# Performance work log

Hardware: AMD Instinct MI355X
Metric: run time of the kernel (lower is better)

Reference implementation:

```python
import jax, jax.numpy as jnp
import numpy as np

NUM_USERS = 100000
NUM_ITEMS = 50000
N_NODES = NUM_USERS + NUM_ITEMS
D = 64
N_LAYERS = 3
E = 2000000
B = 1024
ALPHA_PREF = 1.0


def setup_inputs() -> dict:
    key = jax.random.key(0)
    k1, k2, k3, k4 = jax.random.split(key, 4)
    embed = jax.random.normal(k1, (N_NODES, D), dtype=jnp.float32) * 0.1
    edge_index = jax.random.randint(k2, (2, E), 0, N_NODES, dtype=jnp.int32)
    users = jax.random.randint(k3, (B,), 0, NUM_USERS, dtype=jnp.int32)
    items = jax.random.randint(k4, (B,), 0, NUM_ITEMS, dtype=jnp.int32)
    return {"embed": embed, "edge_index": edge_index, "users": users, "items": items}


def _lightgcn_propagate(x, row, col, norm):
    # message: norm * x[row] (x_j = source), aggregated (add) at col (target)
    msg = norm[:, None] * x[row]                      # [E, D]
    return jnp.zeros_like(x).at[col].add(msg)         # [N, D]


def reference(embed, edge_index, users, items):
    row, col = edge_index[0], edge_index[1]
    n = embed.shape[0]
    # degree normalization (depends only on edge_index; same every layer)
    deg = jnp.zeros((n,), jnp.float32).at[row].add(1.0)
    deg_inv = jnp.clip(deg, 1.0, None) ** -0.5
    norm = deg_inv[row] * deg_inv[col]                # [E]

    x = embed
    for _ in range(N_LAYERS):
        x = _lightgcn_propagate(x, row, col, norm)

    u_emb = x[users]                                  # [B, D]
    i_emb = x[items + NUM_USERS]                      # [B, D]

    # mask = (row == users[:,None]) flattened selection of col; edge e is
    # selected once per batch element b with users[b] == row[e] -> multiplicity
    cnt = jnp.zeros((n,), jnp.float32).at[users].add(1.0)
    mult = cnt[row]                                   # [E] selection multiplicity

    # PreferenceShapley surrogate: softmax over selected neighbor embeddings
    # of alpha_pref * <neigh_emb, mean(u_emb)>, flattened over the batch.
    context = u_emb.mean(0)                           # [D]
    neigh = x[col]                                    # [E, D]
    logits = ALPHA_PREF * (neigh @ context)           # [E]
    masked = jnp.where(mult > 0, logits, -jnp.inf)
    mx = jnp.max(masked)
    ew = mult * jnp.exp(logits - mx)                  # [E] weighted exp (0 where unselected)
    z = jnp.clip(ew.sum(), 1e-12, None)
    neigh_aggr = (ew[:, None] * neigh).sum(0) / z     # [D]

    score = (u_emb * i_emb).sum(-1) + u_emb @ neigh_aggr  # [B]
    return jax.nn.sigmoid(score)
```

## Files before the change

kernel.cpp:

```cpp
#include <hip/hip_runtime.h>
#include <float.h>
#include <math.h>

#define NUM_USERS 100000
#define NUM_ITEMS 50000
#define NNODES    150000
#define DIM       64
#define NEDGE     2000000
#define BATCH     1024
#define SEL_CAP   (1 << 18)
#define LOGIT_BLOCKS 512

#define SLICES   1024
#define EPS      1956
#define NBUK     293
#define BCAP     8192
#define SCAP     16
#define OVF_CAP  4096

__device__ __forceinline__ float wave_sum64(float v) {
    #pragma unroll
    for (int off = 32; off > 0; off >>= 1) v += __shfl_xor(v, off, 64);
    return v;
}

__device__ __forceinline__ float bf2f(unsigned short s) {
    return __uint_as_float(((unsigned int)s) << 16);
}
__device__ __forceinline__ unsigned short f2bf(float f) {
    unsigned int u = __float_as_uint(f);
    return (unsigned short)((u + 0x7fffu + ((u >> 16) & 1u)) >> 16);
}


__global__ __launch_bounds__(512) void sort_kernel(
        const int* __restrict__ row, const int* __restrict__ col,
        const int* __restrict__ ucnt,
        unsigned char* __restrict__ cntC8, unsigned char* __restrict__ cntR8,
        unsigned int* __restrict__ midC2, unsigned short* __restrict__ midR2,
        uint2* __restrict__ ovfC, unsigned int* __restrict__ ovfR,
        int* __restrict__ novfC_g, int* __restrict__ novfR_g,
        int* __restrict__ n_sel, int* __restrict__ sel_col, float* __restrict__ sel_w) {
    __shared__ unsigned int hc[NBUK], hr[NBUK];
    __shared__ unsigned int   stC[NBUK * SCAP];
    __shared__ unsigned short stR[NBUK * SCAP];
    __shared__ int lcnt, lbase;
    __shared__ int2 buf[256];
    int blk = blockIdx.x, t = threadIdx.x;
    for (int i = t; i < NBUK; i += 512) { hc[i] = 0; hr[i] = 0; }
    if (t == 0) lcnt = 0;
    __syncthreads();
    int e0 = blk * EPS;
    int e1 = e0 + EPS; if (e1 > NEDGE) e1 = NEDGE;
    for (int base = e0 + t * 4; base < e1; base += 2048) {
        if (base + 4 <= e1) {
            int4 r4 = *(const int4*)(row + base);
            int4 c4 = *(const int4*)(col + base);
            #pragma unroll
            for (int q = 0; q < 4; ++q) {
                int c = (q == 0) ? c4.x : (q == 1) ? c4.y : (q == 2) ? c4.z : c4.w;
                int r = (q == 0) ? r4.x : (q == 1) ? r4.y : (q == 2) ? r4.z : r4.w;
                int bc = c >> 9;
                unsigned int kc = atomicAdd(&hc[bc], 1u);
                unsigned int v = ((unsigned int)(c & 511) << 18) | (unsigned int)r;
                if (kc < SCAP) stC[bc * SCAP + kc] = v;
                else { int i = atomicAdd(novfC_g, 1); if (i < OVF_CAP) ovfC[i] = make_uint2((unsigned int)bc, v); }
                int br = r >> 9;
                unsigned int kr = atomicAdd(&hr[br], 1u);
                if (kr < SCAP) stR[br * SCAP + kr] = (unsigned short)(r & 511);
                else { int i = atomicAdd(novfR_g, 1); if (i < OVF_CAP) ovfR[i] = ((unsigned int)br << 9) | (unsigned int)(r & 511); }
                int u = ucnt[r];
                if (u > 0) { int i = atomicAdd(&lcnt, 1); if (i < 256) buf[i] = make_int2(c, u); }
            }
        } else {
            for (int e = base; e < e1; ++e) {
                int r = row[e], c = col[e];
                int bc = c >> 9;
                unsigned int kc = atomicAdd(&hc[bc], 1u);
                unsigned int v = ((unsigned int)(c & 511) << 18) | (unsigned int)r;
                if (kc < SCAP) stC[bc * SCAP + kc] = v;
                else { int i = atomicAdd(novfC_g, 1); if (i < OVF_CAP) ovfC[i] = make_uint2((unsigned int)bc, v); }
                int br = r >> 9;
                unsigned int kr = atomicAdd(&hr[br], 1u);
                if (kr < SCAP) stR[br * SCAP + kr] = (unsigned short)(r & 511);
                else { int i = atomicAdd(novfR_g, 1); if (i < OVF_CAP) ovfR[i] = ((unsigned int)br << 9) | (unsigned int)(r & 511); }
                int u = ucnt[r];
                if (u > 0) { int i = atomicAdd(&lcnt, 1); if (i < 256) buf[i] = make_int2(c, u); }
            }
        }
    }
    __syncthreads();
    for (int j = t; j < NBUK * SCAP; j += 512) {
        int b = j >> 4, k = j & (SCAP - 1);
        unsigned int cc = hc[b]; if (cc > SCAP) cc = SCAP;
        if ((unsigned int)k < cc)
            midC2[(size_t)b * (SLICES * SCAP) + blk * SCAP + k] = stC[j];
        unsigned int cr = hr[b]; if (cr > SCAP) cr = SCAP;
        if ((unsigned int)k < cr)
            midR2[(size_t)b * (SLICES * SCAP) + blk * SCAP + k] = stR[j];
    }
    if (t < NBUK) {
        unsigned int cc = hc[t]; if (cc > SCAP) cc = SCAP;
        unsigned int cr = hr[t]; if (cr > SCAP) cr = SCAP;
        cntC8[(size_t)blk * NBUK + t] = (unsigned char)cc;
        cntR8[(size_t)blk * NBUK + t] = (unsigned char)cr;
    }
    if (t == 0) {
        int c = lcnt; c = c < 256 ? c : 256;
        lbase = atomicAdd(n_sel, c);
    }
    __syncthreads();
    int c = lcnt; c = c < 256 ? c : 256;
    int b = lbase;
    for (int i = t; i < c; i += 512) {
        int o = b + i;
        if (o < SEL_CAP) { sel_col[o] = buf[i].x; sel_w[o] = (float)buf[i].y; }
    }
}


__global__ __launch_bounds__(1024) void bfinal_kernel(
        const unsigned int* __restrict__ midC2, const unsigned char* __restrict__ cntC8,
        const unsigned short* __restrict__ midR2, const unsigned char* __restrict__ cntR8,
        const uint2* __restrict__ ovfC, const unsigned int* __restrict__ ovfR,
        const int* __restrict__ novfC_g, const int* __restrict__ novfR_g,
        const float4* __restrict__ embed,
        int* __restrict__ rptr, int* __restrict__ rend, int* __restrict__ src_sorted,
        float* __restrict__ dinv, float* __restrict__ dinv2,
        uint2* __restrict__ y0) {
    __shared__ int cnt[512], sm[512], cur[512];
    __shared__ unsigned char lcC[SLICES], lcR[SLICES];
    __shared__ float dinvL[512];
    int b = blockIdx.x, t = threadIdx.x;
    if (t < SLICES) {
        lcC[t] = cntC8[(size_t)t * NBUK + b];
        lcR[t] = cntR8[(size_t)t * NBUK + b];
    }
    if (t < 512) cnt[t] = 0;
    __syncthreads();
    size_t cbase = (size_t)b * (SLICES * SCAP);
    for (int j = t; j < SLICES * SCAP; j += 1024) {
        if ((unsigned int)(j & (SCAP - 1)) < (unsigned int)lcC[j >> 4])
            atomicAdd(&cnt[midC2[cbase + j] >> 18], 1);
    }
    int noC = *novfC_g; if (noC > OVF_CAP) noC = OVF_CAP;
    for (int i = t; i < noC; i += 1024)
        if ((int)ovfC[i].x == b) atomicAdd(&cnt[ovfC[i].y >> 18], 1);
    __syncthreads();
    if (t < 512) sm[t] = cnt[t];
    __syncthreads();
    for (int off = 1; off < 512; off <<= 1) {
        int v = 0;
        if (t < 512 && t >= off) v = sm[t - off];
        __syncthreads();
        if (t < 512) sm[t] += v;
        __syncthreads();
    }
    int s0 = b * BCAP;
    if (t < 512) {
        int excl = s0 + sm[t] - cnt[t];
        int n = b * 512 + t;
        if (n < NNODES) { rptr[n] = excl; rend[n] = s0 + sm[t]; }
        cur[t] = excl;
    }
    if (b == 0 && t < 16) y0[(size_t)NNODES * 16 + t] = make_uint2(0u, 0u);
    __syncthreads();
    for (int j = t; j < SLICES * SCAP; j += 1024) {
        if ((unsigned int)(j & (SCAP - 1)) < (unsigned int)lcC[j >> 4]) {
            unsigned int v = midC2[cbase + j];
            int dst = atomicAdd(&cur[v >> 18], 1);
            src_sorted[dst] = (int)(v & 0x3FFFFu);
        }
    }
    for (int i = t; i < noC; i += 1024)
        if ((int)ovfC[i].x == b) {
            unsigned int v = ovfC[i].y;
            int dst = atomicAdd(&cur[v >> 18], 1);
            src_sorted[dst] = (int)(v & 0x3FFFFu);
        }
    __syncthreads();
    if (t < 512) cnt[t] = 0;
    __syncthreads();
    for (int j = t; j < SLICES * SCAP; j += 1024) {
        if ((unsigned int)(j & (SCAP - 1)) < (unsigned int)lcR[j >> 4])
            atomicAdd(&cnt[midR2[cbase + j]], 1);
    }
    int noR = *novfR_g; if (noR > OVF_CAP) noR = OVF_CAP;
    for (int i = t; i < noR; i += 1024) {
        unsigned int pv = ovfR[i];
        if ((int)(pv >> 9) == b) atomicAdd(&cnt[pv & 511u], 1);
    }
    __syncthreads();
    if (t < 512) {
        int n = b * 512 + t;
        if (n < NNODES) {
            float d = fmaxf((float)cnt[t], 1.0f);
            float di = rsqrtf(d);
            dinv[n] = di; dinv2[n] = 1.0f / d;
            dinvL[t] = di;
        }
    }
    __syncthreads();
    int nbase = b * 512;
    int nmax = NNODES - nbase; if (nmax > 512) nmax = 512;
    if (nmax < 0) nmax = 0;
    for (int i = t; i < nmax * 16; i += 1024) {
        int ln = i >> 4, slot = i & 15;
        float d = dinvL[ln];
        float4 v = embed[(size_t)(nbase + ln) * 16 + slot];
        unsigned int w0 = (unsigned int)f2bf(v.x * d) | ((unsigned int)f2bf(v.y * d) << 16);
        unsigned int w1 = (unsigned int)f2bf(v.z * d) | ((unsigned int)f2bf(v.w * d) << 16);
        y0[(size_t)(nbase + ln) * 16 + slot] = make_uint2(w0, w1);
    }
}


#define ACC8(V) do { \
    a0 += __uint_as_float((V).x << 16); a1 += __uint_as_float((V).x & 0xffff0000u); \
    a2 += __uint_as_float((V).y << 16); a3 += __uint_as_float((V).y & 0xffff0000u); \
    a4 += __uint_as_float((V).z << 16); a5 += __uint_as_float((V).z & 0xffff0000u); \
    a6 += __uint_as_float((V).w << 16); a7 += __uint_as_float((V).w & 0xffff0000u); \
} while (0)

__device__ __forceinline__ void prop_node(
        const uint4* __restrict__ x_in, uint4* __restrict__ x_out,
        const int* __restrict__ ptr, const int* __restrict__ rend,
        const int* __restrict__ src,
        const float* __restrict__ scale, int node, int sl) {
    int i = ptr[node], e = rend[node];
    float sc = scale[node];
    float a0 = 0.f, a1 = 0.f, a2 = 0.f, a3 = 0.f;
    float a4 = 0.f, a5 = 0.f, a6 = 0.f, a7 = 0.f;
    int p0, p1, p2, p3;
    if (i + 4 <= e) { p0 = src[i]; p1 = src[i + 1]; p2 = src[i + 2]; p3 = src[i + 3]; }
    while (i + 8 <= e) {
        uint4 w0 = x_in[p0 * 8 + sl];
        uint4 w1 = x_in[p1 * 8 + sl];
        uint4 w2 = x_in[p2 * 8 + sl];
        uint4 w3 = x_in[p3 * 8 + sl];
        p0 = src[i + 4]; p1 = src[i + 5]; p2 = src[i + 6]; p3 = src[i + 7];
        i += 4;
        ACC8(w0); ACC8(w1); ACC8(w2); ACC8(w3);
    }
    if (i + 4 <= e) {
        uint4 w0 = x_in[p0 * 8 + sl];
        uint4 w1 = x_in[p1 * 8 + sl];
        uint4 w2 = x_in[p2 * 8 + sl];
        uint4 w3 = x_in[p3 * 8 + sl];
        i += 4;
        ACC8(w0); ACC8(w1); ACC8(w2); ACC8(w3);
    }
    if (i < e) {
        int q0 = src[i];
        int q1 = (i + 1 < e) ? src[i + 1] : NNODES;
        int q2 = (i + 2 < e) ? src[i + 2] : NNODES;
        uint4 w0 = x_in[q0 * 8 + sl];
        uint4 w1 = x_in[q1 * 8 + sl];
        uint4 w2 = x_in[q2 * 8 + sl];
        ACC8(w0); ACC8(w1); ACC8(w2);
    }
    uint4 o;
    o.x = (unsigned int)f2bf(a0 * sc) | ((unsigned int)f2bf(a1 * sc) << 16);
    o.y = (unsigned int)f2bf(a2 * sc) | ((unsigned int)f2bf(a3 * sc) << 16);
    o.z = (unsigned int)f2bf(a4 * sc) | ((unsigned int)f2bf(a5 * sc) << 16);
    o.w = (unsigned int)f2bf(a6 * sc) | ((unsigned int)f2bf(a7 * sc) << 16);
    x_out[(size_t)node * 8 + sl] = o;
}

__global__ __launch_bounds__(256, 8) void prop_kernel(
        const uint4* __restrict__ x_in, uint4* __restrict__ x_out,
        const int* __restrict__ ptr, const int* __restrict__ rend,
        const int* __restrict__ src,
        const float* __restrict__ scale) {
    int gid  = blockIdx.x * blockDim.x + threadIdx.x;
    int node = gid >> 3;
    int sl   = gid & 7;
    if (node > NNODES) return;
    if (node == NNODES) {
        x_out[(size_t)node * 8 + sl] = make_uint4(0u, 0u, 0u, 0u);
        return;
    }
    prop_node(x_in, x_out, ptr, rend, src, scale, node, sl);
}

__global__ __launch_bounds__(256, 8) void prop_list_kernel(
        const uint4* __restrict__ x_in, uint4* __restrict__ x_out,
        const int* __restrict__ ptr, const int* __restrict__ rend,
        const int* __restrict__ src,
        const float* __restrict__ scale,
        const int* __restrict__ users, const int* __restrict__ items,
        const int* __restrict__ sel_col, const int* __restrict__ n_sel_p) {
    int n = *n_sel_p; if (n > SEL_CAP) n = SEL_CAP;
    int total = (2 * BATCH + n) * 8;
    int nth = gridDim.x * blockDim.x;
    for (int gid = blockIdx.x * blockDim.x + threadIdx.x; gid < total; gid += nth) {
        int li = gid >> 3;
        int sl = gid & 7;
        int node;
        if (li < BATCH) {
            node = users[li];
        } else if (li < 2 * BATCH) {
            node = items[li - BATCH] + NUM_USERS;
        } else {
            node = sel_col[li - 2 * BATCH];
        }
        prop_node(x_in, x_out, ptr, rend, src, scale, node, sl);
    }
}


__global__ void ucnt_kernel(const int* __restrict__ users, int* __restrict__ ucnt) {
    int b = blockIdx.x * blockDim.x + threadIdx.x;
    if (b < BATCH) atomicAdd(&ucnt[users[b]], 1);
}

__global__ __launch_bounds__(256) void ctx_part_kernel(
        const unsigned short* __restrict__ x, const int* __restrict__ users,
        float* __restrict__ ctx) {
    __shared__ float sm[256];
    int lane = threadIdx.x & 63, wl = threadIdx.x >> 6;
    int b0 = blockIdx.x * 16 + wl * 4;
    float acc = 0.0f;
    #pragma unroll
    for (int k = 0; k < 4; ++k)
        acc += bf2f(x[users[b0 + k] * DIM + lane]);
    sm[threadIdx.x] = acc;
    __syncthreads();
    if (wl == 0)
        atomicAdd(&ctx[lane], sm[lane] + sm[64 + lane] + sm[128 + lane] + sm[192 + lane]);
}

__global__ void softmax_kernel(const unsigned short* __restrict__ x,
                               const float* __restrict__ ctx,
                               const int* __restrict__ sel_col,
                               const float* __restrict__ sel_w,
                               const int* __restrict__ n_sel_p,
                               float* __restrict__ S, float* __restrict__ zp) {
    __shared__ float smS[4 * 64];
    __shared__ float smZ[4];
    int lane = threadIdx.x & 63, wl = threadIdx.x >> 6;
    int n = *n_sel_p; if (n > SEL_CAP) n = SEL_CAP;
    float c = ctx[lane] * (1.0f / BATCH);
    float accS = 0.0f, accZ = 0.0f;
    int stride = gridDim.x * 4;
    for (int idx = blockIdx.x * 4 + wl; idx < n; idx += stride) {
        int node = sel_col[idx];
        float xv = bf2f(x[node * DIM + lane]);
        float v = wave_sum64(xv * c);
        float w = sel_w[idx] * __expf(v);
        accS = fmaf(w, xv, accS);
        accZ += w;
    }
    smS[wl * 64 + lane] = accS;
    if (lane == 0) smZ[wl] = accZ;
    __syncthreads();
    if (wl == 0) {
        float s = smS[lane] + smS[64 + lane] + smS[128 + lane] + smS[192 + lane];
        atomicAdd(&S[lane], s);
    }
    if (threadIdx.x == 0) atomicAdd(zp, smZ[0] + smZ[1] + smZ[2] + smZ[3]);
}

__global__ void score_kernel(const unsigned short* __restrict__ x, const int* __restrict__ users,
                             const int* __restrict__ items, const float* __restrict__ S,
                             const float* __restrict__ zp, float* __restrict__ out) {
    int gid = blockIdx.x * blockDim.x + threadIdx.x;
    int b = gid >> 6, lane = gid & 63;
    if (b >= BATCH) return;
    float z = fmaxf(*zp, 1e-12f);
    float na = S[lane] / z;
    int u = users[b], it = items[b] + NUM_USERS;
    float v = bf2f(x[u * DIM + lane]) * (bf2f(x[it * DIM + lane]) + na);
    v = wave_sum64(v);
    if (lane == 0) out[b] = 1.0f / (1.0f + __expf(-v));
}


extern "C" void kernel_launch(void* const* d_in, const int* in_sizes, int n_in,
                              void* d_out, int out_size, void* d_ws, size_t ws_size,
                              hipStream_t stream) {
    const float* embed = (const float*)d_in[0];
    const int*   edge  = (const int*)d_in[1];
    const int*   row   = edge;
    const int*   col   = edge + NEDGE;
    const int*   users = (const int*)d_in[2];
    const int*   items = (const int*)d_in[3];
    float*       out   = (float*)d_out;
    char*        ws    = (char*)d_ws;

    size_t off = 0;
    auto A = [&](size_t bytes) { size_t o = off; off += (bytes + 255) & ~(size_t)255; return o; };
    size_t o_midC2 = A((size_t)NBUK * SLICES * SCAP * 4);
    size_t o_midR2 = A((size_t)NBUK * SLICES * SCAP * 2);
    size_t o_xa    = A((size_t)(NNODES + 1) * DIM * 2);
    size_t o_xb    = A((size_t)(NNODES + 1) * DIM * 2);
    size_t o_src   = A((size_t)NBUK * BCAP * 4);
    size_t o_cntC8 = A((size_t)SLICES * NBUK);
    size_t o_cntR8 = A((size_t)SLICES * NBUK);
    size_t o_ovfC  = A((size_t)OVF_CAP * 8);
    size_t o_ovfR  = A((size_t)OVF_CAP * 4);
    size_t o_selc  = A((size_t)SEL_CAP * 4);
    size_t o_selw  = A((size_t)SEL_CAP * 4);
    size_t o_zero  = off;
    size_t o_ucnt  = A((size_t)NNODES * 4);
    size_t o_misc  = A(1024);
    size_t zero_bytes = off - o_zero;
    size_t o_dinv  = A((size_t)NNODES * 4);
    size_t o_dinv2 = A((size_t)NNODES * 4);
    size_t o_rptr  = A((size_t)NNODES * 4);
    size_t o_rend  = A((size_t)NNODES * 4);

    unsigned int*   midC2 = (unsigned int*)(ws + o_midC2);
    unsigned short* midR2 = (unsigned short*)(ws + o_midR2);
    unsigned short* xa   = (unsigned short*)(ws + o_xa);
    unsigned short* xb   = (unsigned short*)(ws + o_xb);
    int*   srcS  = (int*)(ws + o_src);
    unsigned char* cntC8 = (unsigned char*)(ws + o_cntC8);
    unsigned char* cntR8 = (unsigned char*)(ws + o_cntR8);
    uint2* ovfC  = (uint2*)(ws + o_ovfC);
    unsigned int* ovfR = (unsigned int*)(ws + o_ovfR);
    int*   selc  = (int*)(ws + o_selc);
    float* selw  = (float*)(ws + o_selw);
    int*   ucnt  = (int*)(ws + o_ucnt);
    int*   nsel  = (int*)(ws + o_misc);
    float* zp    = (float*)(ws + o_misc + 8);
    float* S     = (float*)(ws + o_misc + 256);
    float* ctx   = (float*)(ws + o_misc + 512);
    int*   novfC = (int*)(ws + o_misc + 768);
    int*   novfR = (int*)(ws + o_misc + 772);
    float* dinv  = (float*)(ws + o_dinv);
    float* dinv2 = (float*)(ws + o_dinv2);
    int*   rptr  = (int*)(ws + o_rptr);
    int*   rend  = (int*)(ws + o_rend);

    hipMemsetAsync(ws + o_zero, 0, zero_bytes, stream);

    ucnt_kernel<<<(BATCH + 255) / 256, 256, 0, stream>>>(users, ucnt);

    sort_kernel<<<SLICES, 512, 0, stream>>>(row, col, ucnt, cntC8, cntR8,
                                            midC2, midR2, ovfC, ovfR, novfC, novfR,
                                            nsel, selc, selw);
    bfinal_kernel<<<NBUK, 1024, 0, stream>>>(midC2, cntC8, midR2, cntR8,
                                             ovfC, ovfR, novfC, novfR,
                                             (const float4*)embed, rptr, rend, srcS,
                                             dinv, dinv2, (uint2*)xa);

    int prop_blocks = ((NNODES + 1) * 8 + 255) / 256;
    prop_kernel<<<prop_blocks, 256, 0, stream>>>((const uint4*)xa, (uint4*)xb, rptr, rend, srcS, dinv2);
    prop_kernel<<<prop_blocks, 256, 0, stream>>>((const uint4*)xb, (uint4*)xa, rptr, rend, srcS, dinv2);
    prop_list_kernel<<<1024, 256, 0, stream>>>((const uint4*)xa, (uint4*)xb,
                                               rptr, rend, srcS, dinv,
                                               users, items, selc, nsel);

    ctx_part_kernel<<<64, 256, 0, stream>>>(xb, users, ctx);
    softmax_kernel<<<LOGIT_BLOCKS, 256, 0, stream>>>(xb, ctx, selc, selw, nsel, S, zp);

    score_kernel<<<(BATCH * 64 + 255) / 256, 256, 0, stream>>>(xb, users, items, S, zp, out);
}
```

Baseline: 256.1 us.

## Split bucket finalize into col and row halves, stage col entries in LDS

The bucket finalize kernel now launches twice as many blocks. The first half builds the CSR-by-target structure and the second half computes source degrees, normalization and the scaled bf16 initial embeddings, so the two run concurrently instead of serially in one block. The col path also stages the valid midC2 entries in a 32 KB shared buffer during counting, so the scatter pass reads LDS instead of rescanning the sparse global slices. The extra LDS may limit occupancy, and the scatter order now depends on atomic order rather than slice order.

```diff
diff --git a/kernel.cpp b/kernel.cpp
--- a/kernel.cpp
+++ b/kernel.cpp
@@ -129,88 +129,97 @@
         float* __restrict__ dinv, float* __restrict__ dinv2,
         uint2* __restrict__ y0) {
     __shared__ int cnt[512], sm[512], cur[512];
-    __shared__ unsigned char lcC[SLICES], lcR[SLICES];
+    __shared__ unsigned int stage[BCAP];
+    __shared__ int nstage;
+    __shared__ unsigned char lc[SLICES];
     __shared__ float dinvL[512];
-    int b = blockIdx.x, t = threadIdx.x;
-    if (t < SLICES) {
-        lcC[t] = cntC8[(size_t)t * NBUK + b];
-        lcR[t] = cntR8[(size_t)t * NBUK + b];
-    }
-    if (t < 512) cnt[t] = 0;
-    __syncthreads();
-    size_t cbase = (size_t)b * (SLICES * SCAP);
-    for (int j = t; j < SLICES * SCAP; j += 1024) {
-        if ((unsigned int)(j & (SCAP - 1)) < (unsigned int)lcC[j >> 4])
-            atomicAdd(&cnt[midC2[cbase + j] >> 18], 1);
-    }
-    int noC = *novfC_g; if (noC > OVF_CAP) noC = OVF_CAP;
-    for (int i = t; i < noC; i += 1024)
-        if ((int)ovfC[i].x == b) atomicAdd(&cnt[ovfC[i].y >> 18], 1);
-    __syncthreads();
-    if (t < 512) sm[t] = cnt[t];
-    __syncthreads();
-    for (int off = 1; off < 512; off <<= 1) {
-        int v = 0;
-        if (t < 512 && t >= off) v = sm[t - off];
-        __syncthreads();
-        if (t < 512) sm[t] += v;
-        __syncthreads();
-    }
-    int s0 = b * BCAP;
-    if (t < 512) {
-        int excl = s0 + sm[t] - cnt[t];
-        int n = b * 512 + t;
-        if (n < NNODES) { rptr[n] = excl; rend[n] = s0 + sm[t]; }
-        cur[t] = excl;
-    }
-    if (b == 0 && t < 16) y0[(size_t)NNODES * 16 + t] = make_uint2(0u, 0u);
-    __syncthreads();
-    for (int j = t; j < SLICES * SCAP; j += 1024) {
-        if ((unsigned int)(j & (SCAP - 1)) < (unsigned int)lcC[j >> 4]) {
-            unsigned int v = midC2[cbase + j];
+    int bb = blockIdx.x, t = threadIdx.x;
+    if (bb < NBUK) {
+        int b = bb;
+        if (t < SLICES) lc[t] = cntC8[(size_t)t * NBUK + b];
+        if (t < 512) cnt[t] = 0;
+        if (t == 0) nstage = 0;
+        __syncthreads();
+        size_t cbase = (size_t)b * (SLICES * SCAP);
+        for (int j = t; j < SLICES * SCAP; j += 1024) {
+            if ((unsigned int)(j & (SCAP - 1)) < (unsigned int)lc[j >> 4]) {
+                unsigned int v = midC2[cbase + j];
+                atomicAdd(&cnt[v >> 18], 1);
+                int i = atomicAdd(&nstage, 1);
+                if (i < BCAP) stage[i] = v;
+            }
+        }
+        int noC = *novfC_g; if (noC > OVF_CAP) noC = OVF_CAP;
+        for (int i = t; i < noC; i += 1024) {
+            if ((int)ovfC[i].x == b) {
+                unsigned int v = ovfC[i].y;
+                atomicAdd(&cnt[v >> 18], 1);
+                int k = atomicAdd(&nstage, 1);
+                if (k < BCAP) stage[k] = v;
+            }
+        }
+        __syncthreads();
+        if (t < 512) sm[t] = cnt[t];
+        __syncthreads();
+        for (int off = 1; off < 512; off <<= 1) {
+            int v = 0;
+            if (t < 512 && t >= off) v = sm[t - off];
+            __syncthreads();
+            if (t < 512) sm[t] += v;
+            __syncthreads();
+        }
+        int s0 = b * BCAP;
+        if (t < 512) {
+            int excl = s0 + sm[t] - cnt[t];
+            int n = b * 512 + t;
+            if (n < NNODES) { rptr[n] = excl; rend[n] = s0 + sm[t]; }
+            cur[t] = excl;
+        }
+        __syncthreads();
+        int ns = nstage; if (ns > BCAP) ns = BCAP;
+        for (int j = t; j < ns; j += 1024) {
+            unsigned int v = stage[j];
             int dst = atomicAdd(&cur[v >> 18], 1);
             src_sorted[dst] = (int)(v & 0x3FFFFu);
         }
-    }
-    for (int i = t; i < noC; i += 1024)
-        if ((int)ovfC[i].x == b) {
-            unsigned int v = ovfC[i].y;
-            int dst = atomicAdd(&cur[v >> 18], 1);
-            src_sorted[dst] = (int)(v & 0x3FFFFu);
-        }
-    __syncthreads();
-    if (t < 512) cnt[t] = 0;
-    __syncthreads();
-    for (int j = t; j < SLICES * SCAP; j += 1024) {
-        if ((unsigned int)(j & (SCAP - 1)) < (unsigned int)lcR[j >> 4])
-            atomicAdd(&cnt[midR2[cbase + j]], 1);
-    }
-    int noR = *novfR_g; if (noR > OVF_CAP) noR = OVF_CAP;
-    for (int i = t; i < noR; i += 1024) {
-        unsigned int pv = ovfR[i];
-        if ((int)(pv >> 9) == b) atomicAdd(&cnt[pv & 511u], 1);
-    }
-    __syncthreads();
-    if (t < 512) {
-        int n = b * 512 + t;
-        if (n < NNODES) {
-            float d = fmaxf((float)cnt[t], 1.0f);
-            float di = rsqrtf(d);
-            dinv[n] = di; dinv2[n] = 1.0f / d;
-            dinvL[t] = di;
-        }
-    }
-    __syncthreads();
-    int nbase = b * 512;
-    int nmax = NNODES - nbase; if (nmax > 512) nmax = 512;
-    if (nmax < 0) nmax = 0;
-    for (int i = t; i < nmax * 16; i += 1024) {
-        int ln = i >> 4, slot = i & 15;
-        float d = dinvL[ln];
-        float4 v = embed[(size_t)(nbase + ln) * 16 + slot];
-        unsigned int w0 = (unsigned int)f2bf(v.x * d) | ((unsigned int)f2bf(v.y * d) << 16);
-        unsigned int w1 = (unsigned int)f2bf(v.z * d) | ((unsigned int)f2bf(v.w * d) << 16);
-        y0[(size_t)(nbase + ln) * 16 + slot] = make_uint2(w0, w1);
+    } else {
+        int b = bb - NBUK;
+        if (t < SLICES) lc[t] = cntR8[(size_t)t * NBUK + b];
+        if (t < 512) cnt[t] = 0;
+        __syncthreads();
+        size_t cbase = (size_t)b * (SLICES * SCAP);
+        for (int j = t; j < SLICES * SCAP; j += 1024) {
+            if ((unsigned int)(j & (SCAP - 1)) < (unsigned int)lc[j >> 4])
+                atomicAdd(&cnt[midR2[cbase + j]], 1);
+        }
+        int noR = *novfR_g; if (noR > OVF_CAP) noR = OVF_CAP;
+        for (int i = t; i < noR; i += 1024) {
+            unsigned int pv = ovfR[i];
+            if ((int)(pv >> 9) == b) atomicAdd(&cnt[pv & 511u], 1);
+        }
+        if (b == 0 && t < 16) y0[(size_t)NNODES * 16 + t] = make_uint2(0u, 0u);
+        __syncthreads();
+        if (t < 512) {
+            int n = b * 512 + t;
+            if (n < NNODES) {
+                float d = fmaxf((float)cnt[t], 1.0f);
+                float di = rsqrtf(d);
+                dinv[n] = di; dinv2[n] = 1.0f / d;
+                dinvL[t] = di;
+            }
+        }
+        __syncthreads();
+        int nbase = b * 512;
+        int nmax = NNODES - nbase; if (nmax > 512) nmax = 512;
+        if (nmax < 0) nmax = 0;
+        for (int i = t; i < nmax * 16; i += 1024) {
+            int ln = i >> 4, slot = i & 15;
+            float d = dinvL[ln];
+            float4 v = embed[(size_t)(nbase + ln) * 16 + slot];
+            unsigned int w0 = (unsigned int)f2bf(v.x * d) | ((unsigned int)f2bf(v.y * d) << 16);
+            unsigned int w1 = (unsigned int)f2bf(v.z * d) | ((unsigned int)f2bf(v.w * d) << 16);
+            y0[(size_t)(nbase + ln) * 16 + slot] = make_uint2(w0, w1);
+        }
     }
 }
 
@@ -440,10 +449,10 @@
     sort_kernel<<<SLICES, 512, 0, stream>>>(row, col, ucnt, cntC8, cntR8,
                                             midC2, midR2, ovfC, ovfR, novfC, novfR,
                                             nsel, selc, selw);
-    bfinal_kernel<<<NBUK, 1024, 0, stream>>>(midC2, cntC8, midR2, cntR8,
-                                             ovfC, ovfR, novfC, novfR,
-                                             (const float4*)embed, rptr, rend, srcS,
-                                             dinv, dinv2, (uint2*)xa);
+    bfinal_kernel<<<2 * NBUK, 1024, 0, stream>>>(midC2, cntC8, midR2, cntR8,
+                                                 ovfC, ovfR, novfC, novfR,
+                                                 (const float4*)embed, rptr, rend, srcS,
+                                                 dinv, dinv2, (uint2*)xa);
 
     int prop_blocks = ((NNODES + 1) * 8 + 255) / 256;
     prop_kernel<<<prop_blocks, 256, 0, stream>>>((const uint4*)xa, (uint4*)xb, rptr, rend, srcS, dinv2);
```

After: 248.4 us. 1.03x faster.
